# Performance work log

Hardware: AMD Instinct MI355X
Metric: run time of the kernel (lower is better)

The kernel has to match this reference:

```python
import jax, jax.numpy as jnp
import numpy as np

N_ROBOTS = 2048   # N
EMBED = 256       # d (= global_embed_dim)
M_GROUPS = 4096   # M
GROUP_K = 16      # fixed group size K
N_OBS = 64


def setup_inputs() -> dict:
    key = jax.random.key(0)
    ks = jax.random.split(key, 6)
    h = jax.random.normal(ks[0], (N_ROBOTS, EMBED), dtype=jnp.float32)
    attn_rr = jax.random.uniform(ks[1], (N_ROBOTS, N_ROBOTS), dtype=jnp.float32)
    attn_ro = jax.random.uniform(ks[2], (N_ROBOTS, N_OBS), dtype=jnp.float32)
    dist_to_goal = jax.random.uniform(ks[3], (N_ROBOTS,), dtype=jnp.float32)
    clearance = jax.random.uniform(ks[4], (N_ROBOTS,), dtype=jnp.float32)
    groups = jax.random.randint(ks[5], (M_GROUPS, GROUP_K), 0, N_ROBOTS)
    return {"h": h, "attn_rr": attn_rr, "attn_ro": attn_ro,
            "dist_to_goal": dist_to_goal, "clearance": clearance, "groups": groups}


def reference(h, attn_rr, attn_ro, dist_to_goal, clearance, groups):
    n_robots, d = h.shape
    m, k = groups.shape
    dt = h.dtype

    # global embedding = mean of per-robot embeddings (h_glob=None path)
    h_glob = h.mean(axis=0)                                   # (d,)

    # pooled group embedding, mean pooling
    h_g = h[groups].mean(axis=1)                              # (M, d)

    # normalized group size
    size_feat = jnp.full((m, 1), k / 3.0, dtype=dt)

    # A_in: mean attention among distinct-index pairs within group
    sub = attn_rr[groups[:, :, None], groups[:, None, :]]     # (M, K, K)
    neq = (groups[:, :, None] != groups[:, None, :]).astype(dt)
    cnt_in = neq.sum(axis=(1, 2))
    a_in = (sub * neq).sum(axis=(1, 2)) / jnp.maximum(cnt_in, 1.0)

    # unique membership indicator per group (set semantics, like torch's group_set)
    member = jnp.zeros((m, n_robots), dtype=dt).at[
        jnp.arange(m)[:, None], groups].set(1.0)              # (M, N)
    n_out = n_robots - member.sum(axis=1)                     # |outside set|

    # A_out: mean attention from group rows (with multiplicity K) to outside columns
    rows = attn_rr[groups]                                    # (M, K, N)
    out_sum = rows.sum(axis=(1, 2)) - jnp.einsum('mkn,mn->m', rows, member)
    a_out = out_sum / jnp.maximum(k * n_out, 1.0)

    # A_obs: mean attention from group robots to all obstacles
    a_obs = attn_ro[groups].mean(axis=(1, 2))

    attn_stats = jnp.stack([a_in, a_out, a_obs], axis=1)      # (M, 3)

    # extra per-robot feature aggregations: dist_to_goal->mean, clearance->min
    ex_dist = dist_to_goal[groups].mean(axis=1, keepdims=True)
    ex_clr = clearance[groups].min(axis=1, keepdims=True)

    h_glob_b = jnp.broadcast_to(h_glob[None, :], (m, d))
    return jnp.concatenate([h_g, h_glob_b, size_feat, attn_stats, ex_dist, ex_clr], axis=1)
```

## Files before the change

### kernel.cpp

```cpp
#include <hip/hip_runtime.h>
#include <hip/hip_bf16.h>

#define N_ROBOTS 2048
#define EMBED 256
#define M_GROUPS 4096
#define GROUP_K 16
#define N_OBS 64
#define OUT_W 518


__global__ __launch_bounds__(256) void precompute_kernel(
    const float* __restrict__ h,
    const float* __restrict__ attn_rr,
    const float* __restrict__ attn_ro,
    float* __restrict__ ws)
{
    const int b = blockIdx.x;
    const int t = threadIdx.x;

    if (b < N_ROBOTS) {
        const float* row = attn_rr + (size_t)b * N_ROBOTS;
        float s = 0.f;
        #pragma unroll
        for (int i = 0; i < N_ROBOTS / 256; ++i) s += row[t + 256 * i];

        float so = 0.f;
        if (t < N_OBS) so = attn_ro[b * N_OBS + t];

        #pragma unroll
        for (int off = 32; off > 0; off >>= 1) {
            s  += __shfl_down(s,  off);
            so += __shfl_down(so, off);
        }
        __shared__ float lds[8];
        const int wave = t >> 6, lane = t & 63;
        if (lane == 0) { lds[wave] = s; lds[4 + wave] = so; }
        __syncthreads();
        if (t == 0) {
            ws[b]            = lds[0] + lds[1] + lds[2] + lds[3];
            ws[N_ROBOTS + b] = lds[4] + lds[5] + lds[6] + lds[7];
        }
    } else {
        const int bb   = b - N_ROBOTS;
        const int col  = bb * 32 + (t & 31);
        const int chnk = t >> 5;
        float s = 0.f;
        const int r0 = chnk * (N_ROBOTS / 8);
        for (int r = r0; r < r0 + N_ROBOTS / 8; ++r)
            s += h[(size_t)r * EMBED + col];
        __shared__ float hg[8][32];
        hg[chnk][t & 31] = s;
        __syncthreads();
        if (t < 32) {
            float tot = 0.f;
            #pragma unroll
            for (int c = 0; c < 8; ++c) tot += hg[c][t];
            ws[2 * N_ROBOTS + bb * 32 + t] = tot;
        }
    }
}

__global__ __launch_bounds__(256) void group_kernel(
    const float* __restrict__ h,
    const float* __restrict__ attn_rr,
    const float* __restrict__ dist,
    const float* __restrict__ clr,
    const int*   __restrict__ groups,
    const float* __restrict__ ws,
    float* __restrict__ out)
{
    const int m = blockIdx.x;
    const int t = threadIdx.x;

    __shared__ int   g[GROUP_K];
    __shared__ int   uniq[GROUP_K];
    __shared__ float s16[4 * GROUP_K];
    __shared__ float red0[256], red1[256], red2[256];

    if (t < GROUP_K) g[t] = groups[m * GROUP_K + t];
    __syncthreads();

    float hsum = 0.f;
    #pragma unroll
    for (int k = 0; k < GROUP_K; ++k) hsum += h[(size_t)g[k] * EMBED + t];

    const int i = t >> 4, j = t & 15;
    const int gi = g[i], gj = g[j];
    const float v   = attn_rr[(size_t)gi * N_ROBOTS + gj];
    const float neq = (gi != gj) ? 1.f : 0.f;

    if (t < GROUP_K) {
        int u = 1;
        for (int p = 0; p < t; ++p) if (g[p] == g[t]) { u = 0; break; }
        uniq[t] = u;
        const int gt = g[t];
        s16[t]                = ws[gt];
        s16[GROUP_K + t]      = ws[N_ROBOTS + gt];
        s16[2 * GROUP_K + t]  = dist[gt];
        s16[3 * GROUP_K + t]  = clr[gt];
    }
    __syncthreads();

    red0[t] = v * neq;
    red1[t] = neq;
    red2[t] = uniq[j] ? v : 0.f;
    __syncthreads();
    #pragma unroll
    for (int off = 128; off > 0; off >>= 1) {
        if (t < off) {
            red0[t] += red0[t + off];
            red1[t] += red1[t + off];
            red2[t] += red2[t + off];
        }
        __syncthreads();
    }

    const size_t base = (size_t)m * OUT_W;
    out[base + t]         = hsum * (1.f / GROUP_K);
    out[base + EMBED + t] = ws[2 * N_ROBOTS + t] * (1.f / N_ROBOTS);

    if (t == 0) {
        float rr = 0.f, ro = 0.f, ds = 0.f;
        float cm = s16[3 * GROUP_K];
        int ucnt = 0;
        #pragma unroll
        for (int k = 0; k < GROUP_K; ++k) {
            rr += s16[k];
            ro += s16[GROUP_K + k];
            ds += s16[2 * GROUP_K + k];
            cm  = fminf(cm, s16[3 * GROUP_K + k]);
            ucnt += uniq[k];
        }
        const float a_in    = red0[0] / fmaxf(red1[0], 1.f);
        const float n_out   = (float)(N_ROBOTS - ucnt);
        const float out_sum = rr - red2[0];
        const float a_out   = out_sum / fmaxf((float)GROUP_K * n_out, 1.f);
        const float a_obs   = ro * (1.f / (GROUP_K * N_OBS));

        out[base + 512] = (float)GROUP_K / 3.0f;
        out[base + 513] = a_in;
        out[base + 514] = a_out;
        out[base + 515] = a_obs;
        out[base + 516] = ds * (1.f / GROUP_K);
        out[base + 517] = cm;
    }
}

extern "C" void kernel_launch(void* const* d_in, const int* in_sizes, int n_in,
                              void* d_out, int out_size, void* d_ws, size_t ws_size,
                              hipStream_t stream) {
    const float* h       = (const float*)d_in[0];
    const float* attn_rr = (const float*)d_in[1];
    const float* attn_ro = (const float*)d_in[2];
    const float* dist    = (const float*)d_in[3];
    const float* clr     = (const float*)d_in[4];
    const int*   groups  = (const int*)d_in[5];
    float* out = (float*)d_out;
    float* ws  = (float*)d_ws;

    precompute_kernel<<<N_ROBOTS + 8, 256, 0, stream>>>(h, attn_rr, attn_ro, ws);
    group_kernel<<<M_GROUPS, 256, 0, stream>>>(h, attn_rr, dist, clr, groups, ws, out);
}
```

Baseline: 36.87 us.

## Shrink group kernel to one wave with shuffle reductions and vectorized loads

The per-group kernel now runs as a single 64-lane wavefront instead of 256 threads. The shared-memory tree reductions and their barriers are replaced by wave shuffles, and h rows and outputs are read and written as float2. The precompute kernel's row sums now use float4 loads. This removes LDS traffic and many __syncthreads per group, at the cost of more work per lane and fewer threads in flight per block.

```diff
diff --git a/kernel.cpp b/kernel.cpp
--- a/kernel.cpp
+++ b/kernel.cpp
@@ -19,13 +19,12 @@
     const int t = threadIdx.x;
 
     if (b < N_ROBOTS) {
-        const float* row = attn_rr + (size_t)b * N_ROBOTS;
-        float s = 0.f;
-        #pragma unroll
-        for (int i = 0; i < N_ROBOTS / 256; ++i) s += row[t + 256 * i];
+        const float4* row4 = (const float4*)(attn_rr + (size_t)b * N_ROBOTS);
+        const float4 a = row4[t];
+        const float4 c = row4[t + 256];
+        float s = (a.x + a.y) + (a.z + a.w) + (c.x + c.y) + (c.z + c.w);
 
-        float so = 0.f;
-        if (t < N_OBS) so = attn_ro[b * N_OBS + t];
+        float so = (t < N_OBS) ? attn_ro[b * N_OBS + t] : 0.f;
 
         #pragma unroll
         for (int off = 32; off > 0; off >>= 1) {
@@ -60,7 +59,7 @@
     }
 }
 
-__global__ __launch_bounds__(256) void group_kernel(
+__global__ __launch_bounds__(64) void group_kernel(
     const float* __restrict__ h,
     const float* __restrict__ attn_rr,
     const float* __restrict__ dist,
@@ -69,80 +68,95 @@
     const float* __restrict__ ws,
     float* __restrict__ out)
 {
-    const int m = blockIdx.x;
-    const int t = threadIdx.x;
+    const int m    = blockIdx.x;
+    const int lane = threadIdx.x;
 
-    __shared__ int   g[GROUP_K];
-    __shared__ int   uniq[GROUP_K];
-    __shared__ float s16[4 * GROUP_K];
-    __shared__ float red0[256], red1[256], red2[256];
+    __shared__ int   gl[GROUP_K];
+    __shared__ float uql[GROUP_K];
 
-    if (t < GROUP_K) g[t] = groups[m * GROUP_K + t];
+    if (lane < GROUP_K) gl[lane] = groups[m * GROUP_K + lane];
     __syncthreads();
 
-    float hsum = 0.f;
-    #pragma unroll
-    for (int k = 0; k < GROUP_K; ++k) hsum += h[(size_t)g[k] * EMBED + t];
-
-    const int i = t >> 4, j = t & 15;
-    const int gi = g[i], gj = g[j];
-    const float v   = attn_rr[(size_t)gi * N_ROBOTS + gj];
-    const float neq = (gi != gj) ? 1.f : 0.f;
-
-    if (t < GROUP_K) {
-        int u = 1;
-        for (int p = 0; p < t; ++p) if (g[p] == g[t]) { u = 0; break; }
-        uniq[t] = u;
-        const int gt = g[t];
-        s16[t]                = ws[gt];
-        s16[GROUP_K + t]      = ws[N_ROBOTS + gt];
-        s16[2 * GROUP_K + t]  = dist[gt];
-        s16[3 * GROUP_K + t]  = clr[gt];
+    if (lane < GROUP_K) {
+        const int gt = gl[lane];
+        float u = 1.f;
+        for (int p = 0; p < lane; ++p) if (gl[p] == gt) { u = 0.f; break; }
+        uql[lane] = u;
     }
     __syncthreads();
 
-    red0[t] = v * neq;
-    red1[t] = neq;
-    red2[t] = uniq[j] ? v : 0.f;
-    __syncthreads();
+    float2 ha = {0.f, 0.f}, hb = {0.f, 0.f};
     #pragma unroll
-    for (int off = 128; off > 0; off >>= 1) {
-        if (t < off) {
-            red0[t] += red0[t + off];
-            red1[t] += red1[t + off];
-            red2[t] += red2[t + off];
-        }
-        __syncthreads();
+    for (int k = 0; k < GROUP_K; ++k) {
+        const float2* hr = (const float2*)(h + (size_t)gl[k] * EMBED);
+        const float2 x = hr[lane];
+        const float2 y = hr[lane + 64];
+        ha.x += x.x; ha.y += x.y;
+        hb.x += y.x; hb.y += y.y;
+    }
+
+    const int   j  = lane & 15;
+    const int   gj = gl[j];
+    const float uj = uql[j];
+    float s_in = 0.f, s_cnt = 0.f, s_uq = 0.f;
+    #pragma unroll
+    for (int q = 0; q < 4; ++q) {
+        const int gi = gl[(lane >> 4) + 4 * q];
+        const float v = attn_rr[(size_t)gi * N_ROBOTS + gj];
+        if (gi != gj) { s_in += v; s_cnt += 1.f; }
+        s_uq += uj * v;
+    }
+
+    float m_rr = 0.f, m_ro = 0.f, m_ds = 0.f, m_cl = 1e30f, m_uq = 0.f;
+    if (lane < GROUP_K) {
+        const int gt = gl[lane];
+        m_rr = ws[gt];
+        m_ro = ws[N_ROBOTS + gt];
+        m_ds = dist[gt];
+        m_cl = clr[gt];
+        m_uq = uql[lane];
+    }
+    #pragma unroll
+    for (int off = 8; off > 0; off >>= 1) {
+        m_rr += __shfl_down(m_rr, off);
+        m_ro += __shfl_down(m_ro, off);
+        m_ds += __shfl_down(m_ds, off);
+        m_cl  = fminf(m_cl, __shfl_down(m_cl, off));
+        m_uq += __shfl_down(m_uq, off);
+    }
+    #pragma unroll
+    for (int off = 32; off > 0; off >>= 1) {
+        s_in  += __shfl_down(s_in,  off);
+        s_cnt += __shfl_down(s_cnt, off);
+        s_uq  += __shfl_down(s_uq,  off);
     }
 
     const size_t base = (size_t)m * OUT_W;
-    out[base + t]         = hsum * (1.f / GROUP_K);
-    out[base + EMBED + t] = ws[2 * N_ROBOTS + t] * (1.f / N_ROBOTS);
+    float2* out2 = (float2*)(out + base);
+    const float2* wg2 = (const float2*)(ws + 2 * N_ROBOTS);
 
-    if (t == 0) {
-        float rr = 0.f, ro = 0.f, ds = 0.f;
-        float cm = s16[3 * GROUP_K];
-        int ucnt = 0;
-        #pragma unroll
-        for (int k = 0; k < GROUP_K; ++k) {
-            rr += s16[k];
-            ro += s16[GROUP_K + k];
-            ds += s16[2 * GROUP_K + k];
-            cm  = fminf(cm, s16[3 * GROUP_K + k]);
-            ucnt += uniq[k];
-        }
-        const float a_in    = red0[0] / fmaxf(red1[0], 1.f);
-        const float n_out   = (float)(N_ROBOTS - ucnt);
-        const float out_sum = rr - red2[0];
-        const float a_out   = out_sum / fmaxf((float)GROUP_K * n_out, 1.f);
-        const float a_obs   = ro * (1.f / (GROUP_K * N_OBS));
+    float2 r;
+    r.x = ha.x * (1.f / GROUP_K); r.y = ha.y * (1.f / GROUP_K);
+    out2[lane] = r;
+    r.x = hb.x * (1.f / GROUP_K); r.y = hb.y * (1.f / GROUP_K);
+    out2[lane + 64] = r;
+    float2 g0 = wg2[lane], g1 = wg2[lane + 64];
+    g0.x *= (1.f / N_ROBOTS); g0.y *= (1.f / N_ROBOTS);
+    g1.x *= (1.f / N_ROBOTS); g1.y *= (1.f / N_ROBOTS);
+    out2[lane + 128] = g0;
+    out2[lane + 192] = g1;
 
+    if (lane == 0) {
+        const float a_in  = s_in / fmaxf(s_cnt, 1.f);
+        const float n_out = (float)N_ROBOTS - m_uq;
+        const float a_out = (m_rr - s_uq) / fmaxf((float)GROUP_K * n_out, 1.f);
+        const float a_obs = m_ro * (1.f / (GROUP_K * N_OBS));
         out[base + 512] = (float)GROUP_K / 3.0f;
         out[base + 513] = a_in;
         out[base + 514] = a_out;
         out[base + 515] = a_obs;
-        out[base + 516] = ds * (1.f / GROUP_K);
-        out[base + 517] = cm;
+        out[base + 516] = m_ds * (1.f / GROUP_K);
+        out[base + 517] = m_cl;
     }
 }
 
@@ -159,5 +173,5 @@
     float* ws  = (float*)d_ws;
 
     precompute_kernel<<<N_ROBOTS + 8, 256, 0, stream>>>(h, attn_rr, attn_ro, ws);
-    group_kernel<<<M_GROUPS, 256, 0, stream>>>(h, attn_rr, dist, clr, groups, ws, out);
+    group_kernel<<<M_GROUPS, 64, 0, stream>>>(h, attn_rr, dist, clr, groups, ws, out);
 }
```

After: 36.81 us. Within noise of the previous version (-0.2%).
